# Optimization experiments

Measured on AMD Instinct MI355X. Metric: run time of the kernel, lower is better.

The kernel has to match this reference:

```python
import jax, jax.numpy as jnp
import numpy as np

# -------- static graph construction (Traffic4cast-style pixel grid) --------
H, W = 495, 436
N = H * W                    # 215820 nodes
D_NODE, D_EDGE, UNITS = 128, 32, 128
UQ = UNITS // 4              # per-quadrant width (combination='concat')
SCALE = 1.0 / 4.0            # 1/(max_neighbors+1)

def _first_occ_unique(v):
    """tf.unique semantics: unique values in first-occurrence order + idx map."""
    u, first, inv = np.unique(v, return_index=True, return_inverse=True)
    order = np.argsort(first)
    rank = np.empty(len(u), dtype=np.int64)
    rank[order] = np.arange(len(u))
    return u[order], rank[inv]

def _build_graph():
    r, c = np.meshgrid(np.arange(H), np.arange(W), indexing='ij')
    node_loc = np.stack([r.ravel(), c.ravel()], -1).astype(np.int64)
    def grid_edges(r0, r1, c0, c1, dr, dc):
        rr, cc = np.meshgrid(np.arange(r0, r1), np.arange(c0, c1), indexing='ij')
        src = (rr * W + cc).ravel()
        dst = ((rr + dr) * W + (cc + dc)).ravel()
        return np.stack([src, dst], -1).astype(np.int64)
    eis = [grid_edges(1, H, 0, W, -1, 0),   # north
           grid_edges(0, H, 0, W - 1, 0, 1),# east
           grid_edges(0, H - 1, 0, W, 1, 0),# south
           grid_edges(0, H, 1, W, 0, -1)]   # west
    return node_loc, eis

NODE_LOC, EIS = _build_graph()

# --- graph_pooling_2x2 bucketing (col_idx=0): pos_id = (r//2)*half_cols + c//2 ---
_half_cols = NODE_LOC[:, 0].max() + 1
_pos_id = (NODE_LOC // 2 * np.array([_half_cols, 1])).sum(-1)
_, NEW_NODE_IDS = _first_occ_unique(_pos_id)
N_POOLED = int(NEW_NODE_IDS.max()) + 1

# --- remove_duplicate_edges precompute per direction (static, int-only) ---
EDGE_SEG, K_UNIQ, KEEP_IDX, NEW_EIDX = [], [], [], []
for _ei in EIS:
    _pe = NEW_NODE_IDS[_ei]
    _lin = _pe[:, 0] * N + _pe[:, 1]
    _u, _seg = _first_occ_unique(_lin)
    _ne = np.stack([_u // N, _u % N], -1)
    _keep = np.where(_ne[:, 0] != _ne[:, 1])[0]
    EDGE_SEG.append(_seg)
    K_UNIQ.append(len(_u))
    KEEP_IDX.append(_keep)
    NEW_EIDX.append(_ne[_keep])


def setup_inputs() -> dict:
    key = jax.random.key(0)
    ks = jax.random.split(key, 9)
    inp = {
        'x': jax.random.normal(ks[0], (N, D_NODE), dtype=jnp.float32),
        'node_loc': jnp.asarray(NODE_LOC),
        'edge_index_n': jnp.asarray(EIS[0]),
        'edge_index_e': jnp.asarray(EIS[1]),
        'edge_index_s': jnp.asarray(EIS[2]),
        'edge_index_w': jnp.asarray(EIS[3]),
        'edges_n': jax.random.uniform(ks[1], (EIS[0].shape[0], D_EDGE), dtype=jnp.float32),
        'edges_e': jax.random.uniform(ks[2], (EIS[1].shape[0], D_EDGE), dtype=jnp.float32),
        'edges_s': jax.random.uniform(ks[3], (EIS[2].shape[0], D_EDGE), dtype=jnp.float32),
        'edges_w': jax.random.uniform(ks[4], (EIS[3].shape[0], D_EDGE), dtype=jnp.float32),
        'W_emb': jax.random.normal(ks[5], (4, D_NODE, UQ), dtype=jnp.float32) * 0.05,
        'W_edge': jax.random.normal(ks[6], (4, D_EDGE + 2 * UQ, UQ), dtype=jnp.float32) * 0.05,
        'W_node': jax.random.normal(ks[7], (D_NODE + UNITS, UNITS), dtype=jnp.float32) * 0.05,
    }
    return inp


def reference(x, node_loc, edge_index_n, edge_index_e, edge_index_s, edge_index_w,
              edges_n, edges_e, edges_s, edges_w, W_emb, W_edge, W_node):
    n = x.shape[0]
    eis = (edge_index_n, edge_index_e, edge_index_s, edge_index_w)
    efs = (edges_n, edges_e, edges_s, edges_w)
    aggs, quad_edges = [], []
    # GeoQuadrantGCN.call_concat (use_global=False, use_bias=False, relu)
    for q in range(4):
        ei = eis[q]
        xq = jax.nn.relu(x @ W_emb[q])                              # [N, UQ]
        edge_in = jnp.concatenate([efs[q], xq[ei[:, 0]], xq[ei[:, 1]]], axis=-1)
        edge = jax.nn.relu(edge_in @ W_edge[q])                     # [E, UQ]
        aggs.append(jax.ops.segment_sum(edge, ei[:, 1], num_segments=n) * SCALE)
        quad_edges.append(edge)
    x2 = jax.nn.relu(jnp.concatenate([x] + aggs, axis=-1) @ W_node) # [N, UNITS]
    # graph_pooling_2x2
    x_pooled = jax.ops.segment_max(x2, jnp.asarray(NEW_NODE_IDS), num_segments=N_POOLED)
    new_pos = jax.ops.segment_min(node_loc // 2, jnp.asarray(NEW_NODE_IDS), num_segments=N_POOLED)
    new_efeats = [
        jax.ops.segment_max(quad_edges[q], jnp.asarray(EDGE_SEG[q]), num_segments=K_UNIQ[q])[KEEP_IDX[q]]
        for q in range(4)
    ]
    new_eidx = [jnp.asarray(NEW_EIDX[q]) for q in range(4)]
    return (x_pooled, new_pos, *new_eidx, *new_efeats)
```

## Files before the change

kernel.cpp:

```cpp
#include <hip/hip_runtime.h>

#define NN 215820
#define NPOOL 54064
#define KN 53846
#define KE 53816

static constexpr size_t OFF_POS = (size_t)NPOOL * 128;
static constexpr size_t OFF_EIN = OFF_POS + (size_t)NPOOL * 2;
static constexpr size_t OFF_EIE = OFF_EIN + (size_t)KN * 2;
static constexpr size_t OFF_EIS = OFF_EIE + (size_t)KE * 2;
static constexpr size_t OFF_EIW = OFF_EIS + (size_t)KN * 2;
static constexpr size_t OFF_EFN = OFF_EIW + (size_t)KE * 2;
static constexpr size_t OFF_EFE = OFF_EFN + (size_t)KN * 32;
static constexpr size_t OFF_EFS = OFF_EFE + (size_t)KE * 32;
static constexpr size_t OFF_EFW = OFF_EFS + (size_t)KN * 32;

typedef __attribute__((ext_vector_type(8))) short  short8v;
typedef __attribute__((ext_vector_type(4))) float  floatx4;

__device__ __align__(16) unsigned short g_wn_h[128 * 256];
__device__ __align__(16) unsigned short g_wn_l[128 * 256];
__device__ __align__(16) unsigned short g_we_h[128 * 128];
__device__ __align__(16) unsigned short g_we_l[128 * 128];
__device__ __align__(16) unsigned short g_wd_h[128 * 96];
__device__ __align__(16) unsigned short g_wd_l[128 * 96];

__device__ __forceinline__ void bf16split(float x, unsigned short& h,
                                          unsigned short& l) {
  const unsigned int u = __float_as_uint(x);
  h = (unsigned short)(u >> 16);
  const float hf = __uint_as_float(u & 0xffff0000u);
  l = (unsigned short)(__float_as_uint(x - hf) >> 16);
}

__global__ __launch_bounds__(256, 4) void k_xq(const float* __restrict__ x,
                                               float* __restrict__ xq) {
  __shared__ __align__(16) short As_h[128 * 32], As_l[128 * 32];
  __shared__ __align__(16) short Bs_h[128 * 32], Bs_l[128 * 32];
  const int t  = threadIdx.x;
  const int n0 = blockIdx.x * 128;
  const int srow = t >> 1, q0 = t & 1;
  int sn = n0 + srow; if (sn >= NN) sn = NN - 1;
  const float* srcx = x + (size_t)sn * 128;
  const int w = t >> 6, lane = t & 63;
  const int lr = lane & 15, lg = lane >> 4;

  floatx4 acc[2][8];
#pragma unroll
  for (int mi = 0; mi < 2; ++mi)
#pragma unroll
    for (int ni = 0; ni < 8; ++ni) acc[mi][ni] = (floatx4){0.f, 0.f, 0.f, 0.f};

  for (int ks = 0; ks < 4; ++ks) {
    __syncthreads();
#pragma unroll
    for (int cc = 0; cc < 2; ++cc) {
      const int q = q0 + 2 * cc;
      const floatx4 v0 = *(const floatx4*)(srcx + ks * 32 + q * 8);
      const floatx4 v1 = *(const floatx4*)(srcx + ks * 32 + q * 8 + 4);
      short8v hv, lv;
#pragma unroll
      for (int j = 0; j < 4; ++j) {
        unsigned short h, l;
        bf16split(v0[j], h, l); hv[j] = (short)h; lv[j] = (short)l;
        bf16split(v1[j], h, l); hv[4 + j] = (short)h; lv[4 + j] = (short)l;
      }
      const int off = srow * 64 + ((q * 16) ^ ((srow & 3) << 4));
      *(short8v*)((char*)As_h + off) = hv;
      *(short8v*)((char*)As_l + off) = lv;
      const size_t wb = (size_t)srow * 128 + ks * 32 + q * 8;
      *(short8v*)((char*)Bs_h + off) = *(const short8v*)(g_we_h + wb);
      *(short8v*)((char*)Bs_l + off) = *(const short8v*)(g_we_l + wb);
    }
    __syncthreads();
    short8v ah[2], al[2];
#pragma unroll
    for (int mi = 0; mi < 2; ++mi) {
      const int row = (mi ? 64 : 0) + 16 * w + lr;
      const int off = row * 64 + ((lg * 16) ^ ((row & 3) << 4));
      ah[mi] = *(const short8v*)((const char*)As_h + off);
      al[mi] = *(const short8v*)((const char*)As_l + off);
    }
#pragma unroll
    for (int ni = 0; ni < 8; ++ni) {
      const int col = 16 * ni + lr;
      const int off = col * 64 + ((lg * 16) ^ ((col & 3) << 4));
      const short8v bh = *(const short8v*)((const char*)Bs_h + off);
      const short8v bl = *(const short8v*)((const char*)Bs_l + off);
#pragma unroll
      for (int mi = 0; mi < 2; ++mi) {
        acc[mi][ni] = __builtin_amdgcn_mfma_f32_16x16x32_bf16(ah[mi], bh, acc[mi][ni], 0, 0, 0);
        acc[mi][ni] = __builtin_amdgcn_mfma_f32_16x16x32_bf16(ah[mi], bl, acc[mi][ni], 0, 0, 0);
        acc[mi][ni] = __builtin_amdgcn_mfma_f32_16x16x32_bf16(al[mi], bh, acc[mi][ni], 0, 0, 0);
      }
    }
  }
#pragma unroll
  for (int ni = 0; ni < 8; ++ni) {
    const int col = 16 * ni + lr;
    const int qq = col >> 5, u = col & 31;
#pragma unroll
    for (int mi = 0; mi < 2; ++mi) {
      const int nb = n0 + (mi ? 64 : 0) + 16 * w + 4 * lg;
#pragma unroll
      for (int r = 0; r < 4; ++r) {
        const int n = nb + r;
        if (n < NN)
          xq[((size_t)qq * NN + n) * 32 + u] = fmaxf(acc[mi][ni][r], 0.f);
      }
    }
  }
}

__global__ __launch_bounds__(256, 4) void k_node(const float* __restrict__ x,
                                                 const float* __restrict__ agg,
                                                 float* __restrict__ out) {
  __shared__ short As_h[128 * 32], As_l[128 * 32];
  __shared__ short Bs_h[128 * 32], Bs_l[128 * 32];
  const int t   = threadIdx.x;
  const int pr  = blockIdx.y;
  const int pc0 = blockIdx.x * 32;

  const int srow = t >> 1, q0 = t & 1;
  int ra = (srow < 64) ? 2 * pr : 2 * pr + 1; if (ra > 494) ra = 494;
  int ca = 2 * pc0 + (srow & 63);          if (ca > 435) ca = 435;
  const size_t snode = (size_t)ra * 436 + ca;

  const int w = t >> 6, lane = t & 63;
  const int lr = lane & 15, lg = lane >> 4;

  floatx4 acc[2][8];
#pragma unroll
  for (int mi = 0; mi < 2; ++mi)
#pragma unroll
    for (int ni = 0; ni < 8; ++ni) acc[mi][ni] = (floatx4){0.f, 0.f, 0.f, 0.f};

  for (int ks = 0; ks < 8; ++ks) {
    __syncthreads();
    const float* src = (ks < 4) ? (x + snode * 128 + ks * 32)
                                : (agg + snode * 128 + (ks - 4) * 32);
#pragma unroll
    for (int cc = 0; cc < 2; ++cc) {
      const int q = q0 + 2 * cc;
      const floatx4 v0 = *(const floatx4*)(src + q * 8);
      const floatx4 v1 = *(const floatx4*)(src + q * 8 + 4);
      short8v hv, lv;
#pragma unroll
      for (int j = 0; j < 4; ++j) {
        unsigned short h, l;
        bf16split(v0[j], h, l); hv[j] = (short)h; lv[j] = (short)l;
        bf16split(v1[j], h, l); hv[4 + j] = (short)h; lv[4 + j] = (short)l;
      }
      const int off = srow * 64 + ((q * 16) ^ ((srow & 3) << 4));
      *(short8v*)((char*)As_h + off) = hv;
      *(short8v*)((char*)As_l + off) = lv;
      const size_t wb = (size_t)srow * 256 + ks * 32 + q * 8;
      *(short8v*)((char*)Bs_h + off) = *(const short8v*)(g_wn_h + wb);
      *(short8v*)((char*)Bs_l + off) = *(const short8v*)(g_wn_l + wb);
    }
    __syncthreads();
    short8v ah[2], al[2];
#pragma unroll
    for (int mi = 0; mi < 2; ++mi) {
      const int row = (mi ? 64 : 0) + 16 * w + lr;
      const int off = row * 64 + ((lg * 16) ^ ((row & 3) << 4));
      ah[mi] = *(const short8v*)((const char*)As_h + off);
      al[mi] = *(const short8v*)((const char*)As_l + off);
    }
#pragma unroll
    for (int ni = 0; ni < 8; ++ni) {
      const int col = 16 * ni + lr;
      const int off = col * 64 + ((lg * 16) ^ ((col & 3) << 4));
      const short8v bh = *(const short8v*)((const char*)Bs_h + off);
      const short8v bl = *(const short8v*)((const char*)Bs_l + off);
#pragma unroll
      for (int mi = 0; mi < 2; ++mi) {
        acc[mi][ni] = __builtin_amdgcn_mfma_f32_16x16x32_bf16(ah[mi], bh, acc[mi][ni], 0, 0, 0);
        acc[mi][ni] = __builtin_amdgcn_mfma_f32_16x16x32_bf16(ah[mi], bl, acc[mi][ni], 0, 0, 0);
        acc[mi][ni] = __builtin_amdgcn_mfma_f32_16x16x32_bf16(al[mi], bh, acc[mi][ni], 0, 0, 0);
      }
    }
  }
#pragma unroll
  for (int ni = 0; ni < 8; ++ni) {
#pragma unroll
    for (int k = 0; k < 2; ++k) {
      float v = fmaxf(fmaxf(acc[0][ni][2 * k], acc[0][ni][2 * k + 1]),
                      fmaxf(acc[1][ni][2 * k], acc[1][ni][2 * k + 1]));
      v = fmaxf(v, 0.f);
      const int pc = pc0 + 8 * w + 2 * lg + k;
      if (pc < 218) out[((size_t)pr * 218 + pc) * 128 + 16 * ni + lr] = v;
    }
  }
}

__global__ __launch_bounds__(256, 4) void k_edge(
    const float* __restrict__ ef_n, const float* __restrict__ ef_e,
    const float* __restrict__ ef_s, const float* __restrict__ ef_w,
    const float* __restrict__ xq, float* __restrict__ agg,
    float* __restrict__ out) {
  __shared__ __align__(16) short As_h[128 * 32], As_l[128 * 32];
  __shared__ __align__(16) short Bs_h[32 * 32],  Bs_l[32 * 32];
  const int t = threadIdx.x;
  int b = blockIdx.x;

  int q, row = 0, pr = 0, c0;
  const float* ef; float* efb;
  if (b < 1976)        { q = 0; ef = ef_n; efb = out + OFF_EFN;
                         row = b >> 2; c0 = (b & 3) * 128; if (c0 > 308) c0 = 308; }
  else if (b < 3952)   { b -= 1976; q = 2; ef = ef_s; efb = out + OFF_EFS;
                         row = b >> 2; c0 = (b & 3) * 128; if (c0 > 308) c0 = 308; }
  else if (b < 5688)   { b -= 3952; q = 1; ef = ef_e; efb = out + OFF_EFE;
                         pr = b / 7;  c0 = (b - pr * 7) * 64; if (c0 > 371) c0 = 371; }
  else                 { b -= 5688; q = 3; ef = ef_w; efb = out + OFF_EFW;
                         pr = b / 7;  c0 = (b - pr * 7) * 64; if (c0 > 371) c0 = 371; }
  const float* xqq = xq + (size_t)q * NN * 32;

  const int srow = t >> 1, q0 = t & 1;
  const float *base0, *base1, *base2;
  if (q == 0) {
    const int e = row * 436 + c0 + srow;
    base0 = ef  + (size_t)e * 32;
    base1 = xqq + (size_t)(e + 436) * 32;
    base2 = xqq + (size_t)e * 32;
  } else if (q == 2) {
    const int e = row * 436 + c0 + srow;
    base0 = ef  + (size_t)e * 32;
    base1 = xqq + (size_t)e * 32;
    base2 = xqq + (size_t)(e + 436) * 32;
  } else {
    int r = 2 * pr + (srow >> 6); if (r > 494) r = 494;
    const int cc = c0 + (srow & 63);
    if (q == 1) {
      base0 = ef  + ((size_t)r * 435 + cc) * 32;
      base1 = xqq + ((size_t)r * 436 + cc) * 32;
      base2 = base1 + 32;
    } else {
      base0 = ef  + ((size_t)r * 435 + cc) * 32;
      base1 = xqq + ((size_t)r * 436 + cc + 1) * 32;
      base2 = base1 - 32;
    }
  }

  const int w = t >> 6, lane = t & 63;
  const int lr = lane & 15, lg = lane >> 4;

  floatx4 acc[2][2];
#pragma unroll
  for (int mi = 0; mi < 2; ++mi)
#pragma unroll
    for (int ni = 0; ni < 2; ++ni) acc[mi][ni] = (floatx4){0.f, 0.f, 0.f, 0.f};

  for (int kc = 0; kc < 3; ++kc) {
    __syncthreads();
    const float* src = (kc == 0) ? base0 : (kc == 1) ? base1 : base2;
#pragma unroll
    for (int cc = 0; cc < 2; ++cc) {
      const int qch = q0 + 2 * cc;
      const floatx4 v0 = *(const floatx4*)(src + qch * 8);
      const floatx4 v1 = *(const floatx4*)(src + qch * 8 + 4);
      short8v hv, lv;
#pragma unroll
      for (int j = 0; j < 4; ++j) {
        unsigned short h, l;
        bf16split(v0[j], h, l); hv[j] = (short)h; lv[j] = (short)l;
        bf16split(v1[j], h, l); hv[4 + j] = (short)h; lv[4 + j] = (short)l;
      }
      const int off = srow * 64 + ((qch * 16) ^ ((srow & 3) << 4));
      *(short8v*)((char*)As_h + off) = hv;
      *(short8v*)((char*)As_l + off) = lv;
    }
    if (t < 128) {
      const int col = t >> 2, ch = t & 3;
      const size_t wb = (size_t)(q * 32 + col) * 96 + kc * 32 + ch * 8;
      const int off = col * 64 + ((ch * 16) ^ ((col & 3) << 4));
      *(short8v*)((char*)Bs_h + off) = *(const short8v*)(g_wd_h + wb);
      *(short8v*)((char*)Bs_l + off) = *(const short8v*)(g_wd_l + wb);
    }
    __syncthreads();
    short8v ah[2], al[2], bh[2], bl[2];
#pragma unroll
    for (int mi = 0; mi < 2; ++mi) {
      const int rowm = 64 * mi + 16 * w + lr;
      const int off = rowm * 64 + ((lg * 16) ^ ((rowm & 3) << 4));
      ah[mi] = *(const short8v*)((const char*)As_h + off);
      al[mi] = *(const short8v*)((const char*)As_l + off);
    }
#pragma unroll
    for (int ni = 0; ni < 2; ++ni) {
      const int col = 16 * ni + lr;
      const int off = col * 64 + ((lg * 16) ^ ((col & 3) << 4));
      bh[ni] = *(const short8v*)((const char*)Bs_h + off);
      bl[ni] = *(const short8v*)((const char*)Bs_l + off);
    }
#pragma unroll
    for (int ni = 0; ni < 2; ++ni)
#pragma unroll
      for (int mi = 0; mi < 2; ++mi) {
        acc[mi][ni] = __builtin_amdgcn_mfma_f32_16x16x32_bf16(ah[mi], bh[ni], acc[mi][ni], 0, 0, 0);
        acc[mi][ni] = __builtin_amdgcn_mfma_f32_16x16x32_bf16(ah[mi], bl[ni], acc[mi][ni], 0, 0, 0);
        acc[mi][ni] = __builtin_amdgcn_mfma_f32_16x16x32_bf16(al[mi], bh[ni], acc[mi][ni], 0, 0, 0);
      }
  }

  float vv[2][2][4];
#pragma unroll
  for (int mi = 0; mi < 2; ++mi)
#pragma unroll
    for (int ni = 0; ni < 2; ++ni)
#pragma unroll
      for (int r = 0; r < 4; ++r) vv[mi][ni][r] = fmaxf(acc[mi][ni][r], 0.f);

#pragma unroll
  for (int ni = 0; ni < 2; ++ni) {
    const int colo = q * 32 + 16 * ni + lr;
#pragma unroll
    for (int mi = 0; mi < 2; ++mi) {
      size_t dstb;
      if (q == 0)      dstb = (size_t)row * 436 + c0 + 64 * mi + 16 * w + 4 * lg;
      else if (q == 2) dstb = (size_t)(row + 1) * 436 + c0 + 64 * mi + 16 * w + 4 * lg;
      else {
        int r2 = 2 * pr + mi; if (r2 > 494) r2 = 494;
        dstb = (size_t)r2 * 436 + c0 + 16 * w + 4 * lg + (q == 1 ? 1 : 0);
      }
#pragma unroll
      for (int r = 0; r < 4; ++r)
        agg[(dstb + r) * 128 + colo] = vv[mi][ni][r] * 0.25f;
    }
  }

  if (q == 0 || q == 2) {
    if (row & 1) {
      const int krow = row >> 1;
#pragma unroll
      for (int ni = 0; ni < 2; ++ni)
#pragma unroll
        for (int mi = 0; mi < 2; ++mi)
#pragma unroll
          for (int k = 0; k < 2; ++k) {
            const int c = c0 + 64 * mi + 16 * w + 4 * lg + 2 * k;
            const int kidx = krow * 218 + (c >> 1);
            const float val = fmaxf(vv[mi][ni][2 * k], vv[mi][ni][2 * k + 1]);
            efb[(size_t)kidx * 32 + 16 * ni + lr] = val;
          }
    }
  } else {
#pragma unroll
    for (int ni = 0; ni < 2; ++ni)
#pragma unroll
      for (int r = 0; r < 4; ++r) {
        const int jj = 16 * w + 4 * lg + r;
        const int c = c0 + jj + (q == 3 ? 1 : 0);
        const bool kept = (q == 1) ? ((c & 1) == 1) : ((c & 1) == 0);
        if (kept) {
          const int kidx = pr * 217 + (c >> 1) - (q == 3 ? 1 : 0);
          const float val = fmaxf(vv[0][ni][r], vv[1][ni][r]);
          efb[(size_t)kidx * 32 + 16 * ni + lr] = val;
        }
      }
  }
}

__global__ __launch_bounds__(256) void k_misc(float* __restrict__ out,
                                              float* __restrict__ agg,
                                              const float* __restrict__ W_node,
                                              const float* __restrict__ W_emb,
                                              const float* __restrict__ W_edge) {
  int u = blockIdx.x * 256 + threadIdx.x;
  if (u < 436 * 32) {
    agg[((size_t)494 * 436 + (u >> 5)) * 128 + (u & 31)] = 0.f; return;
  }
  u -= 436 * 32;
  if (u < 495 * 32) {
    agg[(size_t)(u >> 5) * 436 * 128 + 32 + (u & 31)] = 0.f; return;
  }
  u -= 495 * 32;
  if (u < 436 * 32) {
    agg[(size_t)(u >> 5) * 128 + 64 + (u & 31)] = 0.f; return;
  }
  u -= 436 * 32;
  if (u < 495 * 32) {
    agg[((size_t)(u >> 5) * 436 + 435) * 128 + 96 + (u & 31)] = 0.f; return;
  }
  u -= 495 * 32;
  if (u < NPOOL * 2) {
    const int p  = u >> 1;
    const int pr = p / 218, pc = p - pr * 218;
    out[OFF_POS + u] = (float)((u & 1) ? pc : pr); return;
  }
  u -= NPOOL * 2;
  if (u < KN * 2) {
    const int e  = u >> 1;
    const int kr = e / 218 + 1, pc = e - (kr - 1) * 218;
    const int s  = kr * 218 + pc;
    out[OFF_EIN + u] = (float)((u & 1) ? (s - 218) : s); return;
  }
  u -= KN * 2;
  if (u < KE * 2) {
    const int e  = u >> 1;
    const int pr = e / 217, jj = e - pr * 217;
    const int s  = pr * 218 + jj;
    out[OFF_EIE + u] = (float)((u & 1) ? (s + 1) : s); return;
  }
  u -= KE * 2;
  if (u < KN * 2) {
    const int e  = u >> 1;
    const int k  = e / 218, pc = e - k * 218;
    const int s  = k * 218 + pc;
    out[OFF_EIS + u] = (float)((u & 1) ? (s + 218) : s); return;
  }
  u -= KN * 2;
  if (u < KE * 2) {
    const int e  = u >> 1;
    const int pr = e / 217, jj = e - pr * 217;
    const int s  = pr * 218 + jj + 1;
    out[OFF_EIW + u] = (float)((u & 1) ? (s - 1) : s); return;
  }
  u -= KE * 2;
  if (u < 256 * 128) {
    const int k = u >> 7, c = u & 127;
    unsigned short h, l;
    bf16split(W_node[u], h, l);
    g_wn_h[(size_t)c * 256 + k] = h;
    g_wn_l[(size_t)c * 256 + k] = l;
    return;
  }
  u -= 256 * 128;
  if (u < 4 * 128 * 32) {
    const int q = u >> 12, k = (u >> 5) & 127, uu = u & 31;
    unsigned short h, l;
    bf16split(W_emb[u], h, l);
    g_we_h[(size_t)(q * 32 + uu) * 128 + k] = h;
    g_we_l[(size_t)(q * 32 + uu) * 128 + k] = l;
    return;
  }
  u -= 4 * 128 * 32;
  if (u < 4 * 96 * 32) {
    const int q = u / 3072, rem = u - q * 3072;
    const int k = rem >> 5, col = rem & 31;
    unsigned short h, l;
    bf16split(W_edge[u], h, l);
    g_wd_h[(size_t)(q * 32 + col) * 96 + k] = h;
    g_wd_l[(size_t)(q * 32 + col) * 96 + k] = l;
  }
}

extern "C" void kernel_launch(void* const* d_in, const int* in_sizes, int n_in,
                              void* d_out, int out_size, void* d_ws, size_t ws_size,
                              hipStream_t stream) {
  const float* x      = (const float*)d_in[0];
  const float* ef_n   = (const float*)d_in[6];
  const float* ef_e   = (const float*)d_in[7];
  const float* ef_s   = (const float*)d_in[8];
  const float* ef_w   = (const float*)d_in[9];
  const float* W_emb  = (const float*)d_in[10];
  const float* W_edge = (const float*)d_in[11];
  const float* W_node = (const float*)d_in[12];
  float* out = (float*)d_out;

  float* xq  = (float*)d_ws;
  float* agg = xq + (size_t)NN * 128;

  const int misc_total = (436 + 495 + 436 + 495) * 32 + NPOOL * 2 +
                         2 * (KN * 2 + KE * 2) + 256 * 128 + 4 * 128 * 32 +
                         4 * 96 * 32;
  k_misc<<<dim3((misc_total + 255) / 256), 256, 0, stream>>>(out, agg, W_node,
                                                             W_emb, W_edge);
  k_xq  <<<dim3((NN + 127) / 128), 256, 0, stream>>>(x, xq);
  k_edge<<<dim3(7424), 256, 0, stream>>>(ef_n, ef_e, ef_s, ef_w,
                                         xq, agg, out);
  k_node<<<dim3(7, 248), 256, 0, stream>>>(x, agg, out);
}
```

Before: 448.8 us.

## Prefetch next K-slice into registers and preload full edge weights in shared memory

In the xq and node GEMM kernels, the global loads for the next K-slice of activations are issued into registers right after the barrier, so they overlap the MFMA work on the current slice. In the edge kernel, all three K-chunks of activations are loaded up front, and the full 32x96 weight tile is staged into shared memory once instead of per chunk. The goal is to hide global memory latency inside the main loops. The cost is more registers and more LDS in the edge kernel, which may reduce occupancy.

After: 450.1 us. Within noise of the previous version (+0.3%).

```diff
diff --git a/kernel.cpp b/kernel.cpp
--- a/kernel.cpp
+++ b/kernel.cpp
@@ -51,19 +51,24 @@
 #pragma unroll
     for (int ni = 0; ni < 8; ++ni) acc[mi][ni] = (floatx4){0.f, 0.f, 0.f, 0.f};
 
+  floatx4 nv[2][2];
+#pragma unroll
+  for (int cc = 0; cc < 2; ++cc) {
+    nv[cc][0] = *(const floatx4*)(srcx + q0 * 8 + cc * 16);
+    nv[cc][1] = *(const floatx4*)(srcx + q0 * 8 + cc * 16 + 4);
+  }
+
   for (int ks = 0; ks < 4; ++ks) {
     __syncthreads();
 #pragma unroll
     for (int cc = 0; cc < 2; ++cc) {
       const int q = q0 + 2 * cc;
-      const floatx4 v0 = *(const floatx4*)(srcx + ks * 32 + q * 8);
-      const floatx4 v1 = *(const floatx4*)(srcx + ks * 32 + q * 8 + 4);
       short8v hv, lv;
 #pragma unroll
       for (int j = 0; j < 4; ++j) {
         unsigned short h, l;
-        bf16split(v0[j], h, l); hv[j] = (short)h; lv[j] = (short)l;
-        bf16split(v1[j], h, l); hv[4 + j] = (short)h; lv[4 + j] = (short)l;
+        bf16split(nv[cc][0][j], h, l); hv[j] = (short)h; lv[j] = (short)l;
+        bf16split(nv[cc][1][j], h, l); hv[4 + j] = (short)h; lv[4 + j] = (short)l;
       }
       const int off = srow * 64 + ((q * 16) ^ ((srow & 3) << 4));
       *(short8v*)((char*)As_h + off) = hv;
@@ -73,6 +78,13 @@
       *(short8v*)((char*)Bs_l + off) = *(const short8v*)(g_we_l + wb);
     }
     __syncthreads();
+    if (ks < 3) {
+#pragma unroll
+      for (int cc = 0; cc < 2; ++cc) {
+        nv[cc][0] = *(const floatx4*)(srcx + (ks + 1) * 32 + q0 * 8 + cc * 16);
+        nv[cc][1] = *(const floatx4*)(srcx + (ks + 1) * 32 + q0 * 8 + cc * 16 + 4);
+      }
+    }
     short8v ah[2], al[2];
 #pragma unroll
     for (int mi = 0; mi < 2; ++mi) {
@@ -125,6 +137,8 @@
   int ra = (srow < 64) ? 2 * pr : 2 * pr + 1; if (ra > 494) ra = 494;
   int ca = 2 * pc0 + (srow & 63);          if (ca > 435) ca = 435;
   const size_t snode = (size_t)ra * 436 + ca;
+  const float* xb   = x   + snode * 128;
+  const float* ab   = agg + snode * 128;
 
   const int w = t >> 6, lane = t & 63;
   const int lr = lane & 15, lg = lane >> 4;
@@ -135,21 +149,24 @@
 #pragma unroll
     for (int ni = 0; ni < 8; ++ni) acc[mi][ni] = (floatx4){0.f, 0.f, 0.f, 0.f};
 
+  floatx4 nv[2][2];
+#pragma unroll
+  for (int cc = 0; cc < 2; ++cc) {
+    nv[cc][0] = *(const floatx4*)(xb + q0 * 8 + cc * 16);
+    nv[cc][1] = *(const floatx4*)(xb + q0 * 8 + cc * 16 + 4);
+  }
+
   for (int ks = 0; ks < 8; ++ks) {
     __syncthreads();
-    const float* src = (ks < 4) ? (x + snode * 128 + ks * 32)
-                                : (agg + snode * 128 + (ks - 4) * 32);
 #pragma unroll
     for (int cc = 0; cc < 2; ++cc) {
       const int q = q0 + 2 * cc;
-      const floatx4 v0 = *(const floatx4*)(src + q * 8);
-      const floatx4 v1 = *(const floatx4*)(src + q * 8 + 4);
       short8v hv, lv;
 #pragma unroll
       for (int j = 0; j < 4; ++j) {
         unsigned short h, l;
-        bf16split(v0[j], h, l); hv[j] = (short)h; lv[j] = (short)l;
-        bf16split(v1[j], h, l); hv[4 + j] = (short)h; lv[4 + j] = (short)l;
+        bf16split(nv[cc][0][j], h, l); hv[j] = (short)h; lv[j] = (short)l;
+        bf16split(nv[cc][1][j], h, l); hv[4 + j] = (short)h; lv[4 + j] = (short)l;
       }
       const int off = srow * 64 + ((q * 16) ^ ((srow & 3) << 4));
       *(short8v*)((char*)As_h + off) = hv;
@@ -159,6 +176,15 @@
       *(short8v*)((char*)Bs_l + off) = *(const short8v*)(g_wn_l + wb);
     }
     __syncthreads();
+    if (ks < 7) {
+      const int kn = ks + 1;
+      const float* src = (kn < 4) ? (xb + kn * 32) : (ab + (kn - 4) * 32);
+#pragma unroll
+      for (int cc = 0; cc < 2; ++cc) {
+        nv[cc][0] = *(const floatx4*)(src + q0 * 8 + cc * 16);
+        nv[cc][1] = *(const floatx4*)(src + q0 * 8 + cc * 16 + 4);
+      }
+    }
     short8v ah[2], al[2];
 #pragma unroll
     for (int mi = 0; mi < 2; ++mi) {
@@ -200,7 +226,7 @@
     const float* __restrict__ xq, float* __restrict__ agg,
     float* __restrict__ out) {
   __shared__ __align__(16) short As_h[128 * 32], As_l[128 * 32];
-  __shared__ __align__(16) short Bs_h[32 * 32],  Bs_l[32 * 32];
+  __shared__ __align__(16) short Bs_h[32 * 96],  Bs_l[32 * 96];
   const int t = threadIdx.x;
   int b = blockIdx.x;
 
@@ -242,6 +268,29 @@
     }
   }
 
+  floatx4 pv[3][2][2];
+#pragma unroll
+  for (int kc = 0; kc < 3; ++kc) {
+    const float* src = (kc == 0) ? base0 : (kc == 1) ? base1 : base2;
+#pragma unroll
+    for (int cc = 0; cc < 2; ++cc) {
+      pv[kc][cc][0] = *(const floatx4*)(src + (q0 + 2 * cc) * 8);
+      pv[kc][cc][1] = *(const floatx4*)(src + (q0 + 2 * cc) * 8 + 4);
+    }
+  }
+#pragma unroll
+  for (int r = 0; r < 3; ++r) {
+    const int g = r * 256 + t;
+    const bool lo = g >= 384;
+    const int f = lo ? g - 384 : g;
+    const int col = f / 12, rem = f - col * 12, kc = rem >> 2, ch = rem & 3;
+    const unsigned short* sp = (lo ? g_wd_l : g_wd_h) +
+                               (size_t)(q * 32 + col) * 96 + kc * 32 + ch * 8;
+    short* dp = lo ? Bs_l : Bs_h;
+    const int off = col * 192 + kc * 64 + ((ch * 16) ^ ((col & 3) << 4));
+    *(short8v*)((char*)dp + off) = *(const short8v*)sp;
+  }
+
   const int w = t >> 6, lane = t & 63;
   const int lr = lane & 15, lg = lane >> 4;
 
@@ -251,31 +300,22 @@
 #pragma unroll
     for (int ni = 0; ni < 2; ++ni) acc[mi][ni] = (floatx4){0.f, 0.f, 0.f, 0.f};
 
+#pragma unroll
   for (int kc = 0; kc < 3; ++kc) {
     __syncthreads();
-    const float* src = (kc == 0) ? base0 : (kc == 1) ? base1 : base2;
 #pragma unroll
     for (int cc = 0; cc < 2; ++cc) {
       const int qch = q0 + 2 * cc;
-      const floatx4 v0 = *(const floatx4*)(src + qch * 8);
-      const floatx4 v1 = *(const floatx4*)(src + qch * 8 + 4);
       short8v hv, lv;
 #pragma unroll
       for (int j = 0; j < 4; ++j) {
         unsigned short h, l;
-        bf16split(v0[j], h, l); hv[j] = (short)h; lv[j] = (short)l;
-        bf16split(v1[j], h, l); hv[4 + j] = (short)h; lv[4 + j] = (short)l;
+        bf16split(pv[kc][cc][0][j], h, l); hv[j] = (short)h; lv[j] = (short)l;
+        bf16split(pv[kc][cc][1][j], h, l); hv[4 + j] = (short)h; lv[4 + j] = (short)l;
       }
       const int off = srow * 64 + ((qch * 16) ^ ((srow & 3) << 4));
       *(short8v*)((char*)As_h + off) = hv;
       *(short8v*)((char*)As_l + off) = lv;
-    }
-    if (t < 128) {
-      const int col = t >> 2, ch = t & 3;
-      const size_t wb = (size_t)(q * 32 + col) * 96 + kc * 32 + ch * 8;
-      const int off = col * 64 + ((ch * 16) ^ ((col & 3) << 4));
-      *(short8v*)((char*)Bs_h + off) = *(const short8v*)(g_wd_h + wb);
-      *(short8v*)((char*)Bs_l + off) = *(const short8v*)(g_wd_l + wb);
     }
     __syncthreads();
     short8v ah[2], al[2], bh[2], bl[2];
@@ -289,7 +329,7 @@
 #pragma unroll
     for (int ni = 0; ni < 2; ++ni) {
       const int col = 16 * ni + lr;
-      const int off = col * 64 + ((lg * 16) ^ ((col & 3) << 4));
+      const int off = col * 192 + kc * 64 + ((lg * 16) ^ ((col & 3) << 4));
       bh[ni] = *(const short8v*)((const char*)Bs_h + off);
       bl[ni] = *(const short8v*)((const char*)Bs_l + off);
     }
```
